# Kernel tuning notes

Measured on AMD Instinct MI355X. Metric: run time of the kernel, lower is better.

## Reference

```python
import jax, jax.numpy as jnp
import numpy as np

N_NODES = 100000
NEG_SLOPE = 0.2  # PyG GATConv default


def _add_self_loops(edge_index, n):
    loop = jnp.arange(n, dtype=edge_index.dtype)
    src = jnp.concatenate([edge_index[0], loop])
    dst = jnp.concatenate([edge_index[1], loop])
    return src, dst


def _gat_conv(x, src, dst, W, a_src, a_dst, b, n):
    h = x @ W                                   # [N, d]
    alpha_src = h @ a_src                        # [N]
    alpha_dst = h @ a_dst                        # [N]
    e = alpha_src[src] + alpha_dst[dst]          # [E]
    e = jnp.where(e >= 0, e, NEG_SLOPE * e)      # LeakyReLU
    # segment softmax over incoming edges of each target node
    m = jax.ops.segment_max(e, dst, num_segments=n)   # every node has a self loop
    ex = jnp.exp(e - m[dst])
    denom = jax.ops.segment_sum(ex, dst, num_segments=n)
    alpha = ex / denom[dst]                      # [E]
    out = jax.ops.segment_sum(h[src] * alpha[:, None], dst, num_segments=n)
    return out + b


def setup_inputs() -> dict:
    key = jax.random.key(0)
    ks = jax.random.split(key, 10)
    num_feat, dim = 14, 16
    E = 3200000
    x = jax.random.normal(ks[0], (N_NODES, num_feat), dtype=jnp.float32)
    edge_index = jax.random.randint(ks[1], (2, E), 0, N_NODES, dtype=jnp.int64)
    s1 = 1.0 / np.sqrt(num_feat)
    s2 = 1.0 / np.sqrt(dim)
    return {
        "x": x,
        "edge_index": edge_index,
        "W1": jax.random.uniform(ks[2], (num_feat, dim), jnp.float32, -s1, s1),
        "a_src1": jax.random.uniform(ks[3], (dim,), jnp.float32, -s2, s2),
        "a_dst1": jax.random.uniform(ks[4], (dim,), jnp.float32, -s2, s2),
        "b1": jnp.zeros((dim,), jnp.float32),
        "W2": jax.random.uniform(ks[5], (dim, dim), jnp.float32, -s2, s2),
        "a_src2": jax.random.uniform(ks[6], (dim,), jnp.float32, -s2, s2),
        "a_dst2": jax.random.uniform(ks[7], (dim,), jnp.float32, -s2, s2),
        "b2": jnp.zeros((dim,), jnp.float32),
    }


def reference(x, edge_index, W1, a_src1, a_dst1, b1, W2, a_src2, a_dst2, b2):
    n = x.shape[0]
    src, dst = _add_self_loops(edge_index, n)
    h = _gat_conv(x, src, dst, W1, a_src1, a_dst1, b1, n)
    h = jax.nn.relu(h)
    # F.dropout in eval mode is identity
    out = _gat_conv(h, src, dst, W2, a_src2, a_dst2, b2, n)
    return out
```

## Files before the change

### kernel.cpp

```cpp
#include <hip/hip_runtime.h>
#include <hip/hip_fp16.h>

static constexpr float SLOPE = 0.2f;

#define NPB 256
#define NBMAX 512
#define CAP 10240
#define EPB 8192

__device__ __forceinline__ unsigned fkey(float f) {
    unsigned u = __float_as_uint(f);
    return (u & 0x80000000u) ? ~u : (u | 0x80000000u);
}
__device__ __forceinline__ float fdekey(unsigned k) {
    unsigned u = (k & 0x80000000u) ? (k & 0x7FFFFFFFu) : ~k;
    return __uint_as_float(u);
}

__device__ __forceinline__ int load_idx(const void* ei, int is64, long long pos) {
    return is64 ? (int)((const long long*)ei)[pos] : ((const int*)ei)[pos];
}

__global__ void zero_kernel(unsigned* __restrict__ gkeys, int* __restrict__ bfill) {
    int t = threadIdx.x;
    if (t < 2) gkeys[t] = 0u;
    for (int i = t; i < NBMAX; i += 256) bfill[i] = 0;
}

__global__ void __launch_bounds__(1024) bin_kernel(
        const void* __restrict__ ei, int* __restrict__ bfill,
        unsigned int* __restrict__ packed, int e, int nb) {
    __shared__ int hist[NBMAX];
    __shared__ int lbase[NBMAX];
    __shared__ int cur[NBMAX];
    __shared__ unsigned staged[EPB];
    __shared__ unsigned short sbkt[EPB];
    __shared__ int sflag;
    int t = threadIdx.x;
    if (t < 64) {
        unsigned hi = ((const unsigned*)ei)[2 * t + 1];
        unsigned long long b = __ballot(hi != 0u);
        if (t == 0) sflag = (b == 0ull) ? 1 : 0;
    }
    if (t < NBMAX) hist[t] = 0;
    __syncthreads();
    int is64 = sflag;
    long long e0 = (long long)blockIdx.x * EPB;
    int cnt = (int)min((long long)EPB, (long long)e - e0);
    int sr[8], dr[8];
    if (!is64 && t * 8 + 7 < cnt) {
        const uint4* ps = (const uint4*)((const int*)ei + e0) + t * 2;
        const uint4* pd = (const uint4*)((const int*)ei + e + e0) + t * 2;
        uint4 s0 = ps[0], s1 = ps[1], d0 = pd[0], d1 = pd[1];
        sr[0] = s0.x; sr[1] = s0.y; sr[2] = s0.z; sr[3] = s0.w;
        sr[4] = s1.x; sr[5] = s1.y; sr[6] = s1.z; sr[7] = s1.w;
        dr[0] = d0.x; dr[1] = d0.y; dr[2] = d0.z; dr[3] = d0.w;
        dr[4] = d1.x; dr[5] = d1.y; dr[6] = d1.z; dr[7] = d1.w;
    } else {
#pragma unroll
        for (int r = 0; r < 8; ++r) {
            int i = t * 8 + r;
            dr[r] = -1;
            if (i < cnt) {
                sr[r] = load_idx(ei, is64, e0 + i);
                dr[r] = load_idx(ei, is64, (long long)e + e0 + i);
            }
        }
    }
#pragma unroll
    for (int r = 0; r < 8; ++r)
        if (dr[r] >= 0) atomicAdd(&hist[dr[r] >> 8], 1);
    __syncthreads();
    int v = (t < NBMAX) ? hist[t] : 0;
    if (t < NBMAX) lbase[t] = v;
    __syncthreads();
    for (int off = 1; off < NBMAX; off <<= 1) {
        int y = (t < NBMAX && t >= off) ? lbase[t - off] : 0;
        __syncthreads();
        if (t < NBMAX) lbase[t] += y;
        __syncthreads();
    }
    if (t < NBMAX) {
        lbase[t] -= v;
        cur[t] = lbase[t];
        hist[t] = (v > 0) ? atomicAdd(&bfill[t], v) : 0;
    }
    __syncthreads();
#pragma unroll
    for (int r = 0; r < 8; ++r) {
        if (dr[r] >= 0) {
            int bk = dr[r] >> 8;
            int lp = atomicAdd(&cur[bk], 1);
            staged[lp] = ((unsigned)(dr[r] & 255) << 17) | (unsigned)sr[r];
            sbkt[lp] = (unsigned short)bk;
        }
    }
    __syncthreads();
    for (int i = t; i < cnt; i += 1024) {
        int bk = sbkt[i];
        int within = hist[bk] + (i - lbase[bk]);
        if (within < CAP)
            packed[(long long)bk * CAP + within] = staged[i];
    }
}

template <int NF>
__global__ void feat_kernel(const float* __restrict__ x, const float* __restrict__ W,
                            const float* __restrict__ avs, const float* __restrict__ avd,
                            float* __restrict__ h, __half* __restrict__ h16,
                            float* __restrict__ as, float* __restrict__ ad,
                            unsigned* __restrict__ gkey, int n) {
    __shared__ float sW[NF * 16];
    __shared__ float sa[32];
    int t = threadIdx.x;
    if (t < NF * 16) sW[t] = W[t];
    if (t < 16) sa[t] = avs[t];
    else if (t < 32) sa[t] = avd[t - 16];
    __syncthreads();
    int nid = blockIdx.x * blockDim.x + t;
    if (nid >= n) return;
    float xi[NF];
#pragma unroll
    for (int f = 0; f < NF; ++f) xi[f] = x[(long long)nid * NF + f];
    float hv[16];
    float s1 = 0.f, s2 = 0.f;
#pragma unroll
    for (int k = 0; k < 16; ++k) {
        float acc = 0.f;
#pragma unroll
        for (int f = 0; f < NF; ++f) acc = fmaf(xi[f], sW[f * 16 + k], acc);
        hv[k] = acc;
        s1 = fmaf(acc, sa[k], s1);
        s2 = fmaf(acc, sa[16 + k], s2);
    }
    float4* hp = (float4*)(h + (long long)nid * 16);
    hp[0] = make_float4(hv[0], hv[1], hv[2], hv[3]);
    hp[1] = make_float4(hv[4], hv[5], hv[6], hv[7]);
    hp[2] = make_float4(hv[8], hv[9], hv[10], hv[11]);
    hp[3] = make_float4(hv[12], hv[13], hv[14], hv[15]);
    unsigned u[8];
#pragma unroll
    for (int q = 0; q < 8; ++q) {
        __half2 p2 = __halves2half2(__float2half(hv[2 * q]), __float2half(hv[2 * q + 1]));
        u[q] = *(unsigned*)&p2;
    }
    uint4* hp16 = (uint4*)(h16 + (long long)nid * 16);
    hp16[0] = make_uint4(u[0], u[1], u[2], u[3]);
    hp16[1] = make_uint4(u[4], u[5], u[6], u[7]);
    as[nid] = s1;
    ad[nid] = s2;
}

__global__ void __launch_bounds__(1024) aggr_kernel(
        const float* __restrict__ h, const __half* __restrict__ h16,
        const float* __restrict__ as, const float* __restrict__ ad,
        const unsigned* __restrict__ packed, const int* __restrict__ bfill,
        const float* __restrict__ bias,
        float* __restrict__ out, int n, int do_relu) {
    __shared__ unsigned long long accS[NPB * 9];
    __shared__ unsigned maxS[NPB];
    __shared__ float ccS[NPB];
    __shared__ float adnS[NPB];
    int b = blockIdx.x, t = threadIdx.x;
    int cnt = min(bfill[b], CAP);
    long long pb = (long long)b * CAP;
    if (t < NPB) {
        int node = b * NPB + t;
        float adn = (node < n) ? ad[node] : 0.f;
        adnS[t] = adn;
        float es = (node < n) ? (as[node] + adn) : 0.f;
        es = fmaxf(es, SLOPE * es);
        maxS[t] = fkey(es);
    }
    __syncthreads();
    unsigned pk[10];
    float ev[10];
#pragma unroll
    for (int r = 0; r < 10; ++r) {
        int j = t + r * 1024;
        pk[r] = 0xFFFFFFFFu;
        if (j < cnt) {
            unsigned p = packed[pb + j];
            int dl = p >> 17;
            int s = (int)(p & 0x1FFFF);
            float e2 = as[s] + adnS[dl];
            e2 = fmaxf(e2, SLOPE * e2);
            pk[r] = p;
            ev[r] = e2;
            atomicMax(&maxS[dl], fkey(e2));
        }
    }
    __syncthreads();
    if (t < NPB) {
        int node = b * NPB + t;
        if (node < n) {
            float m = fdekey(maxS[t]);
            float cc = 21.f * 0.69314718f - m;
            ccS[t] = cc;
            float es = as[node] + adnS[t];
            es = fmaxf(es, SLOPE * es);
            float ws = __expf(es + cc);
            unsigned wsi = (unsigned)(int)ws;
            int base = t * 9;
            const float4* hp = (const float4*)(h + (long long)node * 16);
            float4 h0 = hp[0], h1v = hp[1], h2v = hp[2], h3v = hp[3];
            float hv[16] = {h0.x, h0.y, h0.z, h0.w, h1v.x, h1v.y, h1v.z, h1v.w,
                            h2v.x, h2v.y, h2v.z, h2v.w, h3v.x, h3v.y, h3v.z, h3v.w};
#pragma unroll
            for (int q = 0; q < 8; ++q) {
                int t0 = (int)(ws * hv[2 * q]);
                int t1 = (int)(ws * hv[2 * q + 1]);
                accS[base + q] = ((unsigned long long)(unsigned)t1 << 32) +
                                 (unsigned long long)((unsigned)t0 + 0x80000000u);
            }
            accS[base + 8] = (1ull << 32) | wsi;
        }
    }
    __syncthreads();
#pragma unroll
    for (int r = 0; r < 10; ++r) {
        if (pk[r] != 0xFFFFFFFFu) {
            unsigned p = pk[r];
            int dl = p >> 17;
            int s = (int)(p & 0x1FFFF);
            float w = __expf(ev[r] + ccS[dl]);
            unsigned wi = (unsigned)(int)w;
            int base = dl * 9;
            atomicAdd(&accS[base + 8], (1ull << 32) | wi);
            const uint4* hr = (const uint4*)(h16 + (long long)s * 16);
            uint4 r0 = hr[0], r1 = hr[1];
            unsigned rr[8] = {r0.x, r0.y, r0.z, r0.w, r1.x, r1.y, r1.z, r1.w};
#pragma unroll
            for (int q = 0; q < 8; ++q) {
                float2 f = __half22float2(*(__half2*)&rr[q]);
                int t0 = (int)(w * f.x);
                int t1 = (int)(w * f.y);
                unsigned long long enc =
                    ((unsigned long long)(unsigned)t1 << 32) +
                    (unsigned long long)((unsigned)t0 + 0x80000000u);
                atomicAdd(&accS[base + q], enc);
            }
        }
    }
    __syncthreads();
    for (int idx = t; idx < NPB * 16; idx += 1024) {
        int i = idx >> 4, k = idx & 15;
        int node = b * NPB + i;
        if (node < n) {
            unsigned long long dpack = accS[i * 9 + 8];
            unsigned kcnt = (unsigned)(dpack >> 32);
            float den = (float)(unsigned)dpack;
            unsigned long long a = accS[i * 9 + (k >> 1)];
            unsigned lo = (unsigned)a, hi = (unsigned)(a >> 32);
            int s0 = (int)(lo - (kcnt << 31));
            float val;
            if ((k & 1) == 0) {
                val = (float)s0;
            } else {
                long long carries =
                    ((((long long)kcnt) << 31) + (long long)s0) >> 32;
                int s1 = (int)(hi - (unsigned)carries);
                val = (float)s1;
            }
            float o = val / den + bias[k];
            if (do_relu) o = fmaxf(o, 0.f);
            out[(long long)node * 16 + k] = o;
        }
    }
}

extern "C" void kernel_launch(void* const* d_in, const int* in_sizes, int n_in,
                              void* d_out, int out_size, void* d_ws, size_t ws_size,
                              hipStream_t stream) {
    const float* x  = (const float*)d_in[0];
    const void*  ei = d_in[1];
    const float* W1  = (const float*)d_in[2];
    const float* as1 = (const float*)d_in[3];
    const float* ad1 = (const float*)d_in[4];
    const float* b1  = (const float*)d_in[5];
    const float* W2  = (const float*)d_in[6];
    const float* as2 = (const float*)d_in[7];
    const float* ad2 = (const float*)d_in[8];
    const float* b2  = (const float*)d_in[9];
    float* out = (float*)d_out;

    const int n = in_sizes[0] / 14;
    const int e = in_sizes[1] / 2;
    const int nb = (n + NPB - 1) / NPB;

    char* p = (char*)d_ws;
    auto alloc = [&](size_t bytes) {
        char* r = p;
        p += (bytes + 255) & ~(size_t)255;
        return r;
    };
    unsigned* gkeys  = (unsigned*)alloc(256);
    int*      bfill  = (int*)alloc(NBMAX * 4);
    unsigned* packed = (unsigned*)alloc((size_t)nb * CAP * 4);
    float*    h      = (float*)alloc((size_t)n * 16 * 4);
    __half*   h16    = (__half*)alloc((size_t)n * 16 * 2);
    float*    h1     = (float*)alloc((size_t)n * 16 * 4);
    float*    asb    = (float*)alloc((size_t)n * 4);
    float*    adb    = (float*)alloc((size_t)n * 4);

    zero_kernel<<<1, 256, 0, stream>>>(gkeys, bfill);
    bin_kernel<<<(e + EPB - 1) / EPB, 1024, 0, stream>>>(ei, bfill, packed, e, nb);

    feat_kernel<14><<<(n + 255) / 256, 256, 0, stream>>>(x, W1, as1, ad1, h, h16, asb, adb, gkeys + 0, n);
    aggr_kernel<<<nb, 1024, 0, stream>>>(h, h16, asb, adb, packed, bfill, b1, h1, n, 1);
    feat_kernel<16><<<(n + 255) / 256, 256, 0, stream>>>(h1, W2, as2, ad2, h, h16, asb, adb, gkeys + 1, n);
    aggr_kernel<<<nb, 1024, 0, stream>>>(h, h16, asb, adb, packed, bfill, b2, gkeys + 1 ? out : out, n, 0);
}
```

Before: 120.8 us.

## Sort edges by destination in LDS and accumulate per-thread runs before atomics

In the aggregation kernel, edges within each bucket are counting-sorted by local destination node in shared memory. Each thread then processes a contiguous strided run and accumulates in registers, flushing to shared accumulators only when the destination changes. This is meant to cut the shared-memory 64-bit atomic traffic per edge. It adds a histogram, a prefix scan, an extra scatter pass and about 40KB more LDS. The binning kernel is also retuned to 512 threads with 4096 edges per block, and the unused gkey parameter is removed from feat_kernel.

```diff
diff --git a/kernel.cpp b/kernel.cpp
--- a/kernel.cpp
+++ b/kernel.cpp
@@ -6,7 +6,7 @@
 #define NPB 256
 #define NBMAX 512
 #define CAP 10240
-#define EPB 8192
+#define EPB 4096
 
 __device__ __forceinline__ unsigned fkey(float f) {
     unsigned u = __float_as_uint(f);
@@ -27,7 +27,7 @@
     for (int i = t; i < NBMAX; i += 256) bfill[i] = 0;
 }
 
-__global__ void __launch_bounds__(1024) bin_kernel(
+__global__ void __launch_bounds__(512) bin_kernel(
         const void* __restrict__ ei, int* __restrict__ bfill,
         unsigned int* __restrict__ packed, int e, int nb) {
     __shared__ int hist[NBMAX];
@@ -96,7 +96,7 @@
         }
     }
     __syncthreads();
-    for (int i = t; i < cnt; i += 1024) {
+    for (int i = t; i < cnt; i += 512) {
         int bk = sbkt[i];
         int within = hist[bk] + (i - lbase[bk]);
         if (within < CAP)
@@ -108,8 +108,7 @@
 __global__ void feat_kernel(const float* __restrict__ x, const float* __restrict__ W,
                             const float* __restrict__ avs, const float* __restrict__ avd,
                             float* __restrict__ h, __half* __restrict__ h16,
-                            float* __restrict__ as, float* __restrict__ ad,
-                            unsigned* __restrict__ gkey, int n) {
+                            float* __restrict__ as, float* __restrict__ ad, int n) {
     __shared__ float sW[NF * 16];
     __shared__ float sa[32];
     int t = threadIdx.x;
@@ -161,6 +160,9 @@
     __shared__ unsigned maxS[NPB];
     __shared__ float ccS[NPB];
     __shared__ float adnS[NPB];
+    __shared__ int histN[NPB];
+    __shared__ int curN[NPB];
+    __shared__ unsigned sorted[10 * 1026];
     int b = blockIdx.x, t = threadIdx.x;
     int cnt = min(bfill[b], CAP);
     long long pb = (long long)b * CAP;
@@ -171,13 +173,13 @@
         float es = (node < n) ? (as[node] + adn) : 0.f;
         es = fmaxf(es, SLOPE * es);
         maxS[t] = fkey(es);
+        histN[t] = 0;
     }
     __syncthreads();
     unsigned pk[10];
-    float ev[10];
 #pragma unroll
     for (int r = 0; r < 10; ++r) {
-        int j = t + r * 1024;
+        int j = t + (r << 10);
         pk[r] = 0xFFFFFFFFu;
         if (j < cnt) {
             unsigned p = packed[pb + j];
@@ -186,12 +188,22 @@
             float e2 = as[s] + adnS[dl];
             e2 = fmaxf(e2, SLOPE * e2);
             pk[r] = p;
-            ev[r] = e2;
             atomicMax(&maxS[dl], fkey(e2));
-        }
-    }
-    __syncthreads();
+            atomicAdd(&histN[dl], 1);
+        }
+    }
+    __syncthreads();
+    int v = (t < NPB) ? histN[t] : 0;
+    if (t < NPB) curN[t] = v;
+    __syncthreads();
+    for (int off = 1; off < NPB; off <<= 1) {
+        int y = (t < NPB && t >= off) ? curN[t - off] : 0;
+        __syncthreads();
+        if (t < NPB) curN[t] += y;
+        __syncthreads();
+    }
     if (t < NPB) {
+        curN[t] -= v;
         int node = b * NPB + t;
         if (node < n) {
             float m = fdekey(maxS[t]);
@@ -221,26 +233,54 @@
     for (int r = 0; r < 10; ++r) {
         if (pk[r] != 0xFFFFFFFFu) {
             unsigned p = pk[r];
-            int dl = p >> 17;
-            int s = (int)(p & 0x1FFFF);
-            float w = __expf(ev[r] + ccS[dl]);
-            unsigned wi = (unsigned)(int)w;
-            int base = dl * 9;
-            atomicAdd(&accS[base + 8], (1ull << 32) | wi);
-            const uint4* hr = (const uint4*)(h16 + (long long)s * 16);
-            uint4 r0 = hr[0], r1 = hr[1];
-            unsigned rr[8] = {r0.x, r0.y, r0.z, r0.w, r1.x, r1.y, r1.z, r1.w};
-#pragma unroll
-            for (int q = 0; q < 8; ++q) {
-                float2 f = __half22float2(*(__half2*)&rr[q]);
-                int t0 = (int)(w * f.x);
-                int t1 = (int)(w * f.y);
-                unsigned long long enc =
-                    ((unsigned long long)(unsigned)t1 << 32) +
-                    (unsigned long long)((unsigned)t0 + 0x80000000u);
-                atomicAdd(&accS[base + q], enc);
+            int pos = atomicAdd(&curN[p >> 17], 1);
+            int q = pos / 10;
+            int i = pos - q * 10;
+            sorted[q + i * 1026] = p;
+        }
+    }
+    __syncthreads();
+    unsigned long long racc[8] = {0, 0, 0, 0, 0, 0, 0, 0};
+    unsigned long long rden = 0;
+    int curdl = -1;
+    int lim = min(10, cnt - t * 10);
+    for (int i = 0; i < lim; ++i) {
+        unsigned p = sorted[t + i * 1026];
+        int dl = p >> 17;
+        int s = (int)(p & 0x1FFFF);
+        if (dl != curdl) {
+            if (curdl >= 0) {
+                int base = curdl * 9;
+                atomicAdd(&accS[base + 8], rden);
+#pragma unroll
+                for (int q = 0; q < 8; ++q) atomicAdd(&accS[base + q], racc[q]);
             }
-        }
+            curdl = dl;
+            rden = 0;
+#pragma unroll
+            for (int q = 0; q < 8; ++q) racc[q] = 0;
+        }
+        float e2 = as[s] + adnS[dl];
+        e2 = fmaxf(e2, SLOPE * e2);
+        float w = __expf(e2 + ccS[dl]);
+        rden += (1ull << 32) | (unsigned)(int)w;
+        const uint4* hr = (const uint4*)(h16 + (long long)s * 16);
+        uint4 r0 = hr[0], r1 = hr[1];
+        unsigned rr[8] = {r0.x, r0.y, r0.z, r0.w, r1.x, r1.y, r1.z, r1.w};
+#pragma unroll
+        for (int q = 0; q < 8; ++q) {
+            float2 f = __half22float2(*(__half2*)&rr[q]);
+            int t0 = (int)(w * f.x);
+            int t1 = (int)(w * f.y);
+            racc[q] += ((unsigned long long)(unsigned)t1 << 32) +
+                       (unsigned long long)((unsigned)t0 + 0x80000000u);
+        }
+    }
+    if (curdl >= 0) {
+        int base = curdl * 9;
+        atomicAdd(&accS[base + 8], rden);
+#pragma unroll
+        for (int q = 0; q < 8; ++q) atomicAdd(&accS[base + q], racc[q]);
     }
     __syncthreads();
     for (int idx = t; idx < NPB * 16; idx += 1024) {
@@ -304,10 +344,10 @@
     float*    adb    = (float*)alloc((size_t)n * 4);
 
     zero_kernel<<<1, 256, 0, stream>>>(gkeys, bfill);
-    bin_kernel<<<(e + EPB - 1) / EPB, 1024, 0, stream>>>(ei, bfill, packed, e, nb);
-
-    feat_kernel<14><<<(n + 255) / 256, 256, 0, stream>>>(x, W1, as1, ad1, h, h16, asb, adb, gkeys + 0, n);
+    bin_kernel<<<(e + EPB - 1) / EPB, 512, 0, stream>>>(ei, bfill, packed, e, nb);
+
+    feat_kernel<14><<<(n + 255) / 256, 256, 0, stream>>>(x, W1, as1, ad1, h, h16, asb, adb, n);
     aggr_kernel<<<nb, 1024, 0, stream>>>(h, h16, asb, adb, packed, bfill, b1, h1, n, 1);
-    feat_kernel<16><<<(n + 255) / 256, 256, 0, stream>>>(h1, W2, as2, ad2, h, h16, asb, adb, gkeys + 1, n);
-    aggr_kernel<<<nb, 1024, 0, stream>>>(h, h16, asb, adb, packed, bfill, b2, gkeys + 1 ? out : out, n, 0);
-}
+    feat_kernel<16><<<(n + 255) / 256, 256, 0, stream>>>(h1, W2, as2, ad2, h, h16, asb, adb, n);
+    aggr_kernel<<<nb, 1024, 0, stream>>>(h, h16, asb, adb, packed, bfill, b2, out, n, 0);
+}
```

After: 158.0 us. +30.7%, slower.
